# Optimization experiments

Hardware: AMD Instinct MI355X
Metric: run time of the kernel (lower is better)

## Reference

```python
import jax, jax.numpy as jnp
import numpy as np

NUM_CLASSES = 8192
FEAT_DIM = 256
BATCH = 1024
TEMPERATURE = 0.1
BASE_TEMPERATURE = 0.1
PROTO_M = 0.5
EPS = 1e-12  # F.normalize eps


def setup_inputs() -> dict:
    key = jax.random.key(0)
    k1, k2, k3 = jax.random.split(key, 3)
    features = jax.random.normal(k1, (BATCH, FEAT_DIM), dtype=jnp.float32)
    proto = jax.random.normal(k2, (NUM_CLASSES, FEAT_DIM), dtype=jnp.float32)
    # prototypes buffer is unit-normalized after init_class_prototypes
    proto = proto / jnp.maximum(jnp.linalg.norm(proto, axis=1, keepdims=True), EPS)
    labels = jax.random.randint(k3, (BATCH,), 0, NUM_CLASSES, dtype=jnp.int64)
    return {"features": features, "prototypes": proto, "labels": labels}


def _forward(features, prototypes, labels):
    # Sequential per-sample EMA prototype update (order matters for repeated labels)
    def step(proto, fc):
        f, c = fc
        row = proto[c] * PROTO_M + f * (1.0 - PROTO_M)
        row = row / jnp.maximum(jnp.linalg.norm(row), EPS)
        return proto.at[c].set(row), None

    proto, _ = jax.lax.scan(step, prototypes, (features, labels))

    # Pairwise prototype similarity, masked (off-diagonal) mean of exp, then log
    logits = jnp.matmul(proto, proto.T) / TEMPERATURE          # [C, C]
    C = proto.shape[0]
    mask = 1.0 - jnp.eye(C, dtype=logits.dtype)                # zero diagonal
    neg_sum = jnp.sum(mask * jnp.exp(logits), axis=1)          # [C]
    mean_prob_neg = jnp.log(neg_sum / jnp.sum(mask, axis=1))
    # torch drops NaN rows before mean; nanmean reproduces that
    loss = (TEMPERATURE / BASE_TEMPERATURE) * jnp.nanmean(mean_prob_neg)
    return loss


def reference(features, prototypes, labels):
    return _forward(features, prototypes, labels)
```

## Files before the change

kernel.cpp:

```cpp
#include <hip/hip_runtime.h>
#include <hip/hip_bf16.h>
#include <math.h>

#define NUM_CLASSES 8192
#define FEAT_DIM    256
#define BATCH       1024

typedef long fp8x8;
typedef __attribute__((ext_vector_type(4))) float f32x4;

#define GLD16(gp, lp) __builtin_amdgcn_global_load_lds(                       \
    (const __attribute__((address_space(1))) void*)(gp),                      \
    (__attribute__((address_space(3))) void*)(lp), 16, 0, 0)

__global__ __launch_bounds__(256) void ema_convert_kernel(
    const float* __restrict__ feats, const float* __restrict__ proto,
    const int* __restrict__ labels, unsigned char* __restrict__ P8,
    float* __restrict__ rowsum) {
  __shared__ int lab_s[BATCH];
  const int tid = threadIdx.x;

  ((int4*)lab_s)[tid] = ((const int4*)labels)[tid];
  if (blockIdx.x < 32) rowsum[blockIdx.x * 256 + tid] = 0.0f;
  __syncthreads();

  const int c    = (blockIdx.x << 2) + (tid >> 6);
  const int lane = tid & 63;

  float4 p = ((const float4*)(proto + (size_t)c * FEAT_DIM))[lane];

  const int4 L0 = ((const int4*)lab_s)[lane * 4 + 0];
  const int4 L1 = ((const int4*)lab_s)[lane * 4 + 1];
  const int4 L2 = ((const int4*)lab_s)[lane * 4 + 2];
  const int4 L3 = ((const int4*)lab_s)[lane * 4 + 3];
  unsigned m = 0;
  m |= (L0.x == c) << 0;  m |= (L0.y == c) << 1;
  m |= (L0.z == c) << 2;  m |= (L0.w == c) << 3;
  m |= (L1.x == c) << 4;  m |= (L1.y == c) << 5;
  m |= (L1.z == c) << 6;  m |= (L1.w == c) << 7;
  m |= (L2.x == c) << 8;  m |= (L2.y == c) << 9;
  m |= (L2.z == c) << 10; m |= (L2.w == c) << 11;
  m |= (L3.x == c) << 12; m |= (L3.y == c) << 13;
  m |= (L3.z == c) << 14; m |= (L3.w == c) << 15;

  unsigned long long wm = __ballot(m != 0);
  while (wm) {
    const int src = __ffsll((long long)wm) - 1;
    unsigned mm = __shfl(m, src);
    while (mm) {
      const int j = __ffs(mm) - 1;
      mm &= mm - 1;
      const int t = src * 16 + j;
      float4 f = ((const float4*)(feats + (size_t)t * FEAT_DIM))[lane];
      float4 r;
      r.x = 0.5f * p.x + 0.5f * f.x;
      r.y = 0.5f * p.y + 0.5f * f.y;
      r.z = 0.5f * p.z + 0.5f * f.z;
      r.w = 0.5f * p.w + 0.5f * f.w;
      float ss = r.x * r.x + r.y * r.y + r.z * r.z + r.w * r.w;
#pragma unroll
      for (int off = 32; off; off >>= 1) ss += __shfl_xor(ss, off);
      float inv = 1.0f / fmaxf(sqrtf(ss), 1e-12f);
      p.x = r.x * inv; p.y = r.y * inv; p.z = r.z * inv; p.w = r.w * inv;
    }
    wm &= wm - 1;
  }

  int v = __builtin_amdgcn_cvt_pk_fp8_f32(p.x, p.y, 0, false);
  v = __builtin_amdgcn_cvt_pk_fp8_f32(p.z, p.w, v, true);
  ((int*)(P8 + (size_t)c * FEAT_DIM))[lane] = v;
}

#define BM 128
#define NB (NUM_CLASSES / BM)
#define NTRI (NB * (NB + 1) / 2)
#define NBLK (NTRI / 4)
#define LROW 128

#define WAITV(N)                                                              \
  { asm volatile("s_waitcnt vmcnt(" #N ")" ::: "memory");                     \
    __builtin_amdgcn_sched_barrier(0); }
#define BAR() __builtin_amdgcn_s_barrier()

__global__ __launch_bounds__(256, 2) void gemm_rowsum_kernel(
    const unsigned char* __restrict__ P8, float* __restrict__ rowsum) {
  __shared__ __align__(16) char lds[2][2][BM * LROW];

  const int hw  = blockIdx.x;
  const int bid = (hw & 7) * (NBLK / 8) + (hw >> 3);

  int bi_[4], bj_[4];
  {
    int rem = bid * 4, bi = 0;
    while (rem >= (NB - bi)) { rem -= (NB - bi); ++bi; }
    int bj = bi + rem;
#pragma unroll
    for (int k = 0; k < 4; ++k) {
      bi_[k] = bi; bj_[k] = bj;
      if (bj + 1 < NB) ++bj; else { ++bi; bj = bi; }
    }
  }

  const int tid  = threadIdx.x;
  const int wid  = tid >> 6;
  const int lane = tid & 63;
  const int wm   = wid >> 1;
  const int wn   = wid & 1;

  f32x4 acc[4][4] = {};

  const int rloc = lane >> 3;
  const int csrc = (lane & 7) ^ rloc;

#define STAGE(T, KT, BUF)                                                     \
  {                                                                           \
    const unsigned char* PA_ = P8 + (size_t)(bi_[T] * BM) * FEAT_DIM;         \
    const unsigned char* PB_ = P8 + (size_t)(bj_[T] * BM) * FEAT_DIM;         \
    _Pragma("unroll")                                                         \
    for (int q = 0; q < 4; ++q) {                                             \
      const int L = wid * 4 + q;                                   \
      const int r = L * 8 + rloc;                        \
      const size_t go = (size_t)r * FEAT_DIM + (KT) * 128 + csrc * 16;        \
      GLD16(PA_ + go, &lds[BUF][0][L * 1024]);                                \
      GLD16(PB_ + go, &lds[BUF][1][L * 1024]);                                \
    }                                                                         \
  }

  const int g  = lane >> 4;
  const int rl = lane & 15;

#define COMPUTE(BUF)                                                          \
  {                                                                           \
    const char* As = &lds[BUF][0][0];                                         \
    const char* Bs = &lds[BUF][1][0];                                         \
    _Pragma("unroll")                                                         \
    for (int kk = 0; kk < 4; ++kk) {                                          \
      const int cl = 2 * kk + (g >> 1);                \
      const int ib = (g & 1) * 8;                             \
      fp8x8 a[4], b[4];                                                       \
      _Pragma("unroll")                                                       \
      for (int mi = 0; mi < 4; ++mi) {                                        \
        const int row = wm * 64 + mi * 16 + rl;                               \
        a[mi] = *(const fp8x8*)(As + row * LROW + ((cl ^ (row & 7)) << 4) + ib);\
      }                                                                       \
      _Pragma("unroll")                                                       \
      for (int ni = 0; ni < 4; ++ni) {                                        \
        const int row = wn * 64 + ni * 16 + rl;                               \
        b[ni] = *(const fp8x8*)(Bs + row * LROW + ((cl ^ (row & 7)) << 4) + ib);\
      }                                                                       \
      _Pragma("unroll")                                                       \
      for (int mi = 0; mi < 4; ++mi)                                          \
        _Pragma("unroll")                                                     \
        for (int ni = 0; ni < 4; ++ni)                                        \
          acc[mi][ni] = __builtin_amdgcn_mfma_f32_16x16x32_fp8_fp8(           \
              a[mi], b[ni], acc[mi][ni], 0, 0, 0);                            \
    }                                                                         \
  }

#define EPILOGUE(T)                                                           \
  {                                                                           \
    const int BI = bi_[T], BJ = bj_[T];                                       \
    const bool diag = (BI == BJ);                                             \
    float col[4] = {0.0f, 0.0f, 0.0f, 0.0f};                                  \
    _Pragma("unroll")                                                         \
    for (int mi = 0; mi < 4; ++mi) {                                          \
      const int growb = BI * BM + wm * 64 + mi * 16 + g * 4;                  \
      _Pragma("unroll")                                                       \
      for (int v = 0; v < 4; ++v) {                                           \
        const int grow = growb + v;                                           \
        float rs = 0.0f;                                                      \
        _Pragma("unroll")                                                     \
        for (int ni = 0; ni < 4; ++ni) {                                      \
          const int gcol = BJ * BM + wn * 64 + ni * 16 + rl;                  \
          float e = __expf(10.0f * acc[mi][ni][v]);                           \
          if (diag && grow == gcol) e = 0.0f;                                 \
          rs += e;                                                            \
          col[ni] += e;                                                       \
        }                                                                     \
        rs += __shfl_xor(rs, 1);                                              \
        rs += __shfl_xor(rs, 2);                                              \
        rs += __shfl_xor(rs, 4);                                              \
        rs += __shfl_xor(rs, 8);                                              \
        if (rl == 0) atomicAdd(&rowsum[grow], rs);                            \
      }                                                                       \
    }                                                                         \
    if (!diag) {                                                              \
      _Pragma("unroll")                                                       \
      for (int ni = 0; ni < 4; ++ni) {                                        \
        float cs = col[ni];                                                   \
        cs += __shfl_xor(cs, 16);                                             \
        cs += __shfl_xor(cs, 32);                                             \
        if (g == 0) {                                                         \
          const int gcol = BJ * BM + wn * 64 + ni * 16 + rl;                  \
          atomicAdd(&rowsum[gcol], cs);                                       \
        }                                                                     \
      }                                                                       \
    }                                                                         \
  }

#define ZEROACC()                                                             \
  {                                                                           \
    _Pragma("unroll")                                                         \
    for (int mi = 0; mi < 4; ++mi)                                            \
      _Pragma("unroll")                                                       \
      for (int ni = 0; ni < 4; ++ni)                                          \
        acc[mi][ni] = (f32x4){0.0f, 0.0f, 0.0f, 0.0f};                        \
  }

  STAGE(0, 0, 0);
  STAGE(0, 1, 1);
  WAITV(8); BAR(); COMPUTE(0);              BAR(); STAGE(1, 0, 0);
  WAITV(8); BAR(); COMPUTE(1); EPILOGUE(0); ZEROACC(); BAR(); STAGE(1, 1, 1);
  WAITV(8); BAR(); COMPUTE(0);              BAR(); STAGE(2, 0, 0);
  WAITV(8); BAR(); COMPUTE(1); EPILOGUE(1); ZEROACC(); BAR(); STAGE(2, 1, 1);
  WAITV(8); BAR(); COMPUTE(0);              BAR(); STAGE(3, 0, 0);
  WAITV(8); BAR(); COMPUTE(1); EPILOGUE(2); ZEROACC(); BAR(); STAGE(3, 1, 1);
  WAITV(8); BAR(); COMPUTE(0);              BAR();
  WAITV(0); BAR(); COMPUTE(1); EPILOGUE(3);
}

__global__ __launch_bounds__(256) void finalize_kernel(
    const float* __restrict__ rowsum, float* __restrict__ out) {
  const int tid = threadIdx.x;
  float s = 0.0f;
  for (int i = tid; i < NUM_CLASSES; i += 256) {
    s += logf(rowsum[i] * (1.0f / (float)(NUM_CLASSES - 1)));
  }
#pragma unroll
  for (int off = 32; off; off >>= 1) s += __shfl_xor(s, off);
  __shared__ float red[4];
  if ((tid & 63) == 0) red[tid >> 6] = s;
  __syncthreads();
  if (tid == 0)
    out[0] = (red[0] + red[1] + red[2] + red[3]) * (1.0f / (float)NUM_CLASSES);
}

extern "C" void kernel_launch(void* const* d_in, const int* in_sizes, int n_in,
                              void* d_out, int out_size, void* d_ws, size_t ws_size,
                              hipStream_t stream) {
  const float* feats  = (const float*)d_in[0];
  const float* proto  = (const float*)d_in[1];
  const int*   labels = (const int*)d_in[2];
  float*       out    = (float*)d_out;

  char* ws = (char*)d_ws;
  unsigned char* P8 = (unsigned char*)ws;
  float* rowsum = (float*)(ws + (size_t)NUM_CLASSES * FEAT_DIM);

  ema_convert_kernel<<<NUM_CLASSES / 4, 256, 0, stream>>>(feats, proto, labels,
                                                          P8, rowsum);
  gemm_rowsum_kernel<<<NBLK, 256, 0, stream>>>(P8, rowsum);
  finalize_kernel<<<1, 256, 0, stream>>>(rowsum, out);
}
```

Before: 68.94 us.

## Halve tiles per block, single-buffer LDS, and stage rowsum atomics through LDS

```diff
diff --git a/kernel.cpp b/kernel.cpp
--- a/kernel.cpp
+++ b/kernel.cpp
@@ -74,32 +74,24 @@
 #define BM 128
 #define NB (NUM_CLASSES / BM)
 #define NTRI (NB * (NB + 1) / 2)
-#define NBLK (NTRI / 4)
+#define NBLK (NTRI / 2)
 #define LROW 128
 
-#define WAITV(N)                                                              \
-  { asm volatile("s_waitcnt vmcnt(" #N ")" ::: "memory");                     \
-    __builtin_amdgcn_sched_barrier(0); }
-#define BAR() __builtin_amdgcn_s_barrier()
-
-__global__ __launch_bounds__(256, 2) void gemm_rowsum_kernel(
+__global__ __launch_bounds__(256, 4) void gemm_rowsum_kernel(
     const unsigned char* __restrict__ P8, float* __restrict__ rowsum) {
-  __shared__ __align__(16) char lds[2][2][BM * LROW];
+  __shared__ __align__(16) char As[BM * LROW];
+  __shared__ __align__(16) char Bs[BM * LROW];
+  __shared__ float Lrow[2][2][BM];
+  __shared__ float Lcol[2][2][BM];
 
   const int hw  = blockIdx.x;
   const int bid = (hw & 7) * (NBLK / 8) + (hw >> 3);
 
-  int bi_[4], bj_[4];
-  {
-    int rem = bid * 4, bi = 0;
-    while (rem >= (NB - bi)) { rem -= (NB - bi); ++bi; }
-    int bj = bi + rem;
-#pragma unroll
-    for (int k = 0; k < 4; ++k) {
-      bi_[k] = bi; bj_[k] = bj;
-      if (bj + 1 < NB) ++bj; else { ++bi; bj = bi; }
-    }
-  }
+  int rem = bid * 2, bi0 = 0;
+  while (rem >= (NB - bi0)) { rem -= (NB - bi0); ++bi0; }
+  const int bj0 = bi0 + rem;
+  const int bi1 = (bj0 + 1 < NB) ? bi0 : bi0 + 1;
+  const int bj1 = (bj0 + 1 < NB) ? bj0 + 1 : bi0 + 1;
 
   const int tid  = threadIdx.x;
   const int wid  = tid >> 6;
@@ -111,28 +103,26 @@
 
   const int rloc = lane >> 3;
   const int csrc = (lane & 7) ^ rloc;
-
-#define STAGE(T, KT, BUF)                                                     \
-  {                                                                           \
-    const unsigned char* PA_ = P8 + (size_t)(bi_[T] * BM) * FEAT_DIM;         \
-    const unsigned char* PB_ = P8 + (size_t)(bj_[T] * BM) * FEAT_DIM;         \
+  const unsigned char* PA = P8 + (size_t)(bi0 * BM) * FEAT_DIM;
+  const unsigned char* PB = P8 + (size_t)(bj0 * BM) * FEAT_DIM;
+
+#define STAGE(kt)                                                             \
+  {                                                                           \
     _Pragma("unroll")                                                         \
     for (int q = 0; q < 4; ++q) {                                             \
       const int L = wid * 4 + q;                                   \
       const int r = L * 8 + rloc;                        \
-      const size_t go = (size_t)r * FEAT_DIM + (KT) * 128 + csrc * 16;        \
-      GLD16(PA_ + go, &lds[BUF][0][L * 1024]);                                \
-      GLD16(PB_ + go, &lds[BUF][1][L * 1024]);                                \
+      const size_t go = (size_t)r * FEAT_DIM + (kt) * 128 + csrc * 16;        \
+      GLD16(PA + go, As + L * 1024);                                          \
+      GLD16(PB + go, Bs + L * 1024);                                          \
     }                                                                         \
   }
 
   const int g  = lane >> 4;
   const int rl = lane & 15;
 
-#define COMPUTE(BUF)                                                          \
-  {                                                                           \
-    const char* As = &lds[BUF][0][0];                                         \
-    const char* Bs = &lds[BUF][1][0];                                         \
+#define COMPUTE()                                                             \
+  {                                                                           \
     _Pragma("unroll")                                                         \
     for (int kk = 0; kk < 4; ++kk) {                                          \
       const int cl = 2 * kk + (g >> 1);                \
@@ -157,21 +147,20 @@
     }                                                                         \
   }
 
-#define EPILOGUE(T)                                                           \
-  {                                                                           \
-    const int BI = bi_[T], BJ = bj_[T];                                       \
-    const bool diag = (BI == BJ);                                             \
+#define EPI_CALC(T, BI, BJ)                                                   \
+  {                                                                           \
+    const bool diag = ((BI) == (BJ));                                         \
     float col[4] = {0.0f, 0.0f, 0.0f, 0.0f};                                  \
     _Pragma("unroll")                                                         \
     for (int mi = 0; mi < 4; ++mi) {                                          \
-      const int growb = BI * BM + wm * 64 + mi * 16 + g * 4;                  \
       _Pragma("unroll")                                                       \
       for (int v = 0; v < 4; ++v) {                                           \
-        const int grow = growb + v;                                           \
+        const int lrow = wm * 64 + mi * 16 + g * 4 + v;                       \
+        const int grow = (BI) * BM + lrow;                                    \
         float rs = 0.0f;                                                      \
         _Pragma("unroll")                                                     \
         for (int ni = 0; ni < 4; ++ni) {                                      \
-          const int gcol = BJ * BM + wn * 64 + ni * 16 + rl;                  \
+          const int gcol = (BJ) * BM + wn * 64 + ni * 16 + rl;                \
           float e = __expf(10.0f * acc[mi][ni][v]);                           \
           if (diag && grow == gcol) e = 0.0f;                                 \
           rs += e;                                                            \
@@ -181,20 +170,15 @@
         rs += __shfl_xor(rs, 2);                                              \
         rs += __shfl_xor(rs, 4);                                              \
         rs += __shfl_xor(rs, 8);                                              \
-        if (rl == 0) atomicAdd(&rowsum[grow], rs);                            \
+        if (rl == 0) Lrow[T][wn][lrow] = rs;                                  \
       }                                                                       \
     }                                                                         \
-    if (!diag) {                                                              \
-      _Pragma("unroll")                                                       \
-      for (int ni = 0; ni < 4; ++ni) {                                        \
-        float cs = col[ni];                                                   \
-        cs += __shfl_xor(cs, 16);                                             \
-        cs += __shfl_xor(cs, 32);                                             \
-        if (g == 0) {                                                         \
-          const int gcol = BJ * BM + wn * 64 + ni * 16 + rl;                  \
-          atomicAdd(&rowsum[gcol], cs);                                       \
-        }                                                                     \
-      }                                                                       \
+    _Pragma("unroll")                                                         \
+    for (int ni = 0; ni < 4; ++ni) {                                          \
+      float cs = col[ni];                                                     \
+      cs += __shfl_xor(cs, 16);                                               \
+      cs += __shfl_xor(cs, 32);                                               \
+      if (g == 0) Lcol[T][wm][wn * 64 + ni * 16 + rl] = cs;                   \
     }                                                                         \
   }
 
@@ -207,16 +191,38 @@
         acc[mi][ni] = (f32x4){0.0f, 0.0f, 0.0f, 0.0f};                        \
   }
 
-  STAGE(0, 0, 0);
-  STAGE(0, 1, 1);
-  WAITV(8); BAR(); COMPUTE(0);              BAR(); STAGE(1, 0, 0);
-  WAITV(8); BAR(); COMPUTE(1); EPILOGUE(0); ZEROACC(); BAR(); STAGE(1, 1, 1);
-  WAITV(8); BAR(); COMPUTE(0);              BAR(); STAGE(2, 0, 0);
-  WAITV(8); BAR(); COMPUTE(1); EPILOGUE(1); ZEROACC(); BAR(); STAGE(2, 1, 1);
-  WAITV(8); BAR(); COMPUTE(0);              BAR(); STAGE(3, 0, 0);
-  WAITV(8); BAR(); COMPUTE(1); EPILOGUE(2); ZEROACC(); BAR(); STAGE(3, 1, 1);
-  WAITV(8); BAR(); COMPUTE(0);              BAR();
-  WAITV(0); BAR(); COMPUTE(1); EPILOGUE(3);
+  STAGE(0);
+  __syncthreads();
+
+  COMPUTE();
+  __syncthreads();
+  STAGE(1);
+  __syncthreads();
+  COMPUTE();
+  __syncthreads();
+  PA = P8 + (size_t)(bi1 * BM) * FEAT_DIM;
+  PB = P8 + (size_t)(bj1 * BM) * FEAT_DIM;
+  STAGE(0);
+  EPI_CALC(0, bi0, bj0);
+  ZEROACC();
+  __syncthreads();
+  COMPUTE();
+  __syncthreads();
+  STAGE(1);
+  __syncthreads();
+  COMPUTE();
+  EPI_CALC(1, bi1, bj1);
+  __syncthreads();
+
+  {
+    const int T = tid >> 7;
+    const int r = tid & 127;
+    const int biT = T ? bi1 : bi0;
+    const int bjT = T ? bj1 : bj0;
+    atomicAdd(&rowsum[biT * BM + r], Lrow[T][0][r] + Lrow[T][1][r]);
+    if (biT != bjT)
+      atomicAdd(&rowsum[bjT * BM + r], Lcol[T][0][r] + Lcol[T][1][r]);
+  }
 }
 
 __global__ __launch_bounds__(256) void finalize_kernel(
```

Result: faster. 61.05 us (-11.4%).
